# Kernel optimization log

Hardware: AMD Instinct MI355X
Metric: run time of the kernel (lower is better)

Reference implementation:

```python
import jax, jax.numpy as jnp
import numpy as np

B = 65536  # batch size


def setup_inputs() -> dict:
    key = jax.random.key(0)
    kx, kw, kb = jax.random.split(key, 3)
    x = jax.random.normal(kx, (B, 784), dtype=jnp.float32)
    W = jax.random.normal(kw, (10, 784), dtype=jnp.float32) * 0.03
    b = jax.random.normal(kb, (10,), dtype=jnp.float32) * 0.03
    return {"x": x, "W": W, "b": b}


def _quanv_features(x):
    # x: [B, 784] -> [B, 28, 28] -> 2x2 patches in row-major patch order,
    # each patch flattened as [p(r,c), p(r,c+1), p(r+1,c), p(r+1,c+1)].
    Bn = x.shape[0]
    p = x.reshape(Bn, 14, 2, 14, 2).transpose(0, 1, 3, 2, 4).reshape(Bn, 196, 4)
    # Analytic 4-qubit circuit: RY(x_i)|0>, CNOT(0,1), CNOT(2,3), <Z_i>
    # => [cos x0, cos x0 * cos x1, cos x2, cos x2 * cos x3]
    c = jnp.cos(p)
    m = jnp.stack(
        [c[..., 0], c[..., 0] * c[..., 1], c[..., 2], c[..., 2] * c[..., 3]],
        axis=-1,
    )
    # residual add with the raw patch, then concat over 196 patches -> [B, 784]
    return (m + p).reshape(Bn, 784)


def reference(x, W, b):
    feats = _quanv_features(x)              # [B, 784]
    logits = feats @ W.T + b                # [B, 10]
    return jax.nn.log_softmax(logits, axis=-1)
```

## Files before the change

### kernel.cpp

```cpp
#include <hip/hip_runtime.h>
#include <hip/hip_bf16.h>
#include <stdint.h>


typedef __attribute__((ext_vector_type(8))) short short8;
typedef __attribute__((ext_vector_type(4))) float f32x4;

__global__ void quanv_wprep_kernel(const float* __restrict__ Wm,
                                   uint32_t* __restrict__ ws) {
    const int idx = blockIdx.x * 256 + threadIdx.x;
    if (idx >= 7168) return;
    const int kb   = idx >> 8;
    const int rem  = idx & 255;
    const int l    = rem >> 2;
    const int d    = rem & 3;
    const int n    = l & 15;
    const int kg   = l >> 4;
    const int pr   = kb >> 1;
    const int half = kb & 1;
    uint32_t outv = 0;
    if (n < 10) {
        uint32_t hv[2];
#pragma unroll
        for (int d2 = 0; d2 < 2; ++d2) {
            const int e  = 2 * d + d2;
            const int fi = ((kg >= 2) ? 2 : 0) + (e & 1);
            int j; bool pad = false;
            if (half == 0) {
                j = 4 * (kg & 1) + (e >> 1);
            } else if ((kg & 1) == 0) {
                j = 8 + (e >> 1);
            } else {
                pad = (e < 4);
                const int e4 = (e >= 4) ? (e - 4) : 0;
                j = 12 + (e4 >> 1);
            }
            const float v = pad ? 0.f : Wm[n * 784 + (pr * 14 + j) * 4 + fi];
            hv[d2] = (uint32_t)__bfloat16_as_ushort(__float2bfloat16(v));
        }
        outv = hv[0] | (hv[1] << 16);
    }
    ws[idx] = outv;
}

#define QKB(P, IMM, WF) do {                                                  \
    const float4 va = *(const float4*)((P) + (IMM));                          \
    const float4 vb = *(const float4*)((P) + (IMM) + 4);                      \
    float g0,g1,g2,g3,g4,g5,g6,g7;                                            \
    { const float ce=__cosf(va.x), co=__cosf(va.y);                           \
      g0 = ce + va.x; g1 = fmaf(ce, co, va.y); }                              \
    { const float ce=__cosf(va.z), co=__cosf(va.w);                           \
      g2 = ce + va.z; g3 = fmaf(ce, co, va.w); }                              \
    { const float ce=__cosf(vb.x), co=__cosf(vb.y);                           \
      g4 = ce + vb.x; g5 = fmaf(ce, co, vb.y); }                              \
    { const float ce=__cosf(vb.z), co=__cosf(vb.w);                           \
      g6 = ce + vb.z; g7 = fmaf(ce, co, vb.w); }                              \
    short8 a;                                                                 \
    a[0]=(short)__bfloat16_as_ushort(__float2bfloat16(g0));                   \
    a[1]=(short)__bfloat16_as_ushort(__float2bfloat16(g1));                   \
    a[2]=(short)__bfloat16_as_ushort(__float2bfloat16(g2));                   \
    a[3]=(short)__bfloat16_as_ushort(__float2bfloat16(g3));                   \
    a[4]=(short)__bfloat16_as_ushort(__float2bfloat16(g4));                   \
    a[5]=(short)__bfloat16_as_ushort(__float2bfloat16(g5));                   \
    a[6]=(short)__bfloat16_as_ushort(__float2bfloat16(g6));                   \
    a[7]=(short)__bfloat16_as_ushort(__float2bfloat16(g7));                   \
    acc = __builtin_amdgcn_mfma_f32_16x16x32_bf16(a, (WF), acc, 0, 0, 0);     \
} while (0)

__global__ __launch_bounds__(256, 4)
void quanv_mfma3_kernel(const float* __restrict__ x,
                        const char* __restrict__ wsb,
                        const float* __restrict__ bias,
                        float* __restrict__ out) {
    __shared__ f32x4 red[2][64];

    const int t   = threadIdx.x;
    const int l   = t & 63;
    const int w   = t >> 6;
    const int rg  = __builtin_amdgcn_readfirstlane(w >> 1);
    const int kh  = __builtin_amdgcn_readfirstlane(w & 1);
    const int r16 = l & 15;
    const int kg  = l >> 4;
    const int rowBase = blockIdx.x * 32 + rg * 16;
    const float* xr = x + (size_t)(rowBase + r16) * 784 + kh * 392;

    const int off0 = (kg == 0) ? 0  : (kg == 1) ? 8  : (kg == 2) ? 28 : 36;
    const int off1 = (kg == 0) ? 16 : (kg == 1) ? 20 : (kg == 2) ? 44 : 48;
    const float* p0 = xr + off0;
    const float* p1 = xr + off1;

    const char* wbp = wsb + kh * 14336 + l * 16;
    const short8 wf0  = *(const short8*)(wbp + 0  * 1024);
    const short8 wf1  = *(const short8*)(wbp + 1  * 1024);
    const short8 wf2  = *(const short8*)(wbp + 2  * 1024);
    const short8 wf3  = *(const short8*)(wbp + 3  * 1024);
    const short8 wf4  = *(const short8*)(wbp + 4  * 1024);
    const short8 wf5  = *(const short8*)(wbp + 5  * 1024);
    const short8 wf6  = *(const short8*)(wbp + 6  * 1024);
    const short8 wf7  = *(const short8*)(wbp + 7  * 1024);
    const short8 wf8  = *(const short8*)(wbp + 8  * 1024);
    const short8 wf9  = *(const short8*)(wbp + 9  * 1024);
    const short8 wf10 = *(const short8*)(wbp + 10 * 1024);
    const short8 wf11 = *(const short8*)(wbp + 11 * 1024);
    const short8 wf12 = *(const short8*)(wbp + 12 * 1024);
    const short8 wf13 = *(const short8*)(wbp + 13 * 1024);

    f32x4 acc = {0.f, 0.f, 0.f, 0.f};

    QKB(p0, 0 * 56, wf0);  QKB(p1, 0 * 56, wf1);
    QKB(p0, 1 * 56, wf2);  QKB(p1, 1 * 56, wf3);
    QKB(p0, 2 * 56, wf4);  QKB(p1, 2 * 56, wf5);
    QKB(p0, 3 * 56, wf6);  QKB(p1, 3 * 56, wf7);
    QKB(p0, 4 * 56, wf8);  QKB(p1, 4 * 56, wf9);
    QKB(p0, 5 * 56, wf10); QKB(p1, 5 * 56, wf11);
    QKB(p0, 6 * 56, wf12); QKB(p1, 6 * 56, wf13);

    if (kh == 1) red[rg][l] = acc;
    __syncthreads();
    if (kh == 0) {
        const f32x4 o = red[rg][l];
#pragma unroll
        for (int j = 0; j < 4; ++j) acc[j] += o[j];

        const float bn = bias[r16 < 10 ? r16 : 0];
#pragma unroll
        for (int j = 0; j < 4; ++j) {
            float v = (r16 < 10) ? (acc[j] + bn) : -1e30f;
            float mx = v;
            mx = fmaxf(mx, __shfl_xor(mx, 1, 64));
            mx = fmaxf(mx, __shfl_xor(mx, 2, 64));
            mx = fmaxf(mx, __shfl_xor(mx, 4, 64));
            mx = fmaxf(mx, __shfl_xor(mx, 8, 64));
            float e = (r16 < 10) ? __expf(v - mx) : 0.f;
            float s = e;
            s += __shfl_xor(s, 1, 64);
            s += __shfl_xor(s, 2, 64);
            s += __shfl_xor(s, 4, 64);
            s += __shfl_xor(s, 8, 64);
            const float ls = __logf(s) + mx;
            if (r16 < 10)
                out[(size_t)(rowBase + 4 * kg + j) * 10 + r16] = v - ls;
        }
    }
}

extern "C" void kernel_launch(void* const* d_in, const int* in_sizes, int n_in,
                              void* d_out, int out_size, void* d_ws, size_t ws_size,
                              hipStream_t stream) {
    const float* x    = (const float*)d_in[0];
    const float* Wm   = (const float*)d_in[1];
    const float* bias = (const float*)d_in[2];
    float* out        = (float*)d_out;

    quanv_wprep_kernel<<<dim3(28), dim3(256), 0, stream>>>(
        Wm, (uint32_t*)d_ws);
    quanv_mfma3_kernel<<<dim3(2048), dim3(256), 0, stream>>>(
        x, (const char*)d_ws, bias, out);
}
```

Baseline: 45.92 us.

## Remap K dimension to contiguous 784-element layout removing padded MFMA steps

The K axis is re-indexed so each lane reads contiguous float4 pairs straight from the original row order, with the weight-prep kernel permuting W to match. This cuts the MFMA count from 28 to 25 K-tiles per row group by removing padding, and the tail tile reuses a valid in-row address (px) whose weights are zeroed. The two K-halves become unbalanced (13 vs 12 tiles), and the wider strided access pattern per lane changes coalescing.

```diff
diff --git a/kernel.cpp b/kernel.cpp
--- a/kernel.cpp
+++ b/kernel.cpp
@@ -9,33 +9,29 @@
 __global__ void quanv_wprep_kernel(const float* __restrict__ Wm,
                                    uint32_t* __restrict__ ws) {
     const int idx = blockIdx.x * 256 + threadIdx.x;
-    if (idx >= 7168) return;
-    const int kb   = idx >> 8;
-    const int rem  = idx & 255;
-    const int l    = rem >> 2;
-    const int d    = rem & 3;
-    const int n    = l & 15;
-    const int kg   = l >> 4;
-    const int pr   = kb >> 1;
-    const int half = kb & 1;
+    if (idx >= 6400) return;
+    const int kt  = idx >> 8;
+    const int rem = idx & 255;
+    const int l   = rem >> 2;
+    const int d   = rem & 3;
+    const int n   = l & 15;
+    const int kg  = l >> 4;
     uint32_t outv = 0;
     if (n < 10) {
         uint32_t hv[2];
 #pragma unroll
         for (int d2 = 0; d2 < 2; ++d2) {
             const int e  = 2 * d + d2;
-            const int fi = ((kg >= 2) ? 2 : 0) + (e & 1);
-            int j; bool pad = false;
-            if (half == 0) {
-                j = 4 * (kg & 1) + (e >> 1);
-            } else if ((kg & 1) == 0) {
-                j = 8 + (e >> 1);
-            } else {
-                pad = (e < 4);
-                const int e4 = (e >= 4) ? (e - 4) : 0;
-                j = 12 + (e4 >> 1);
+            const int jp = 32 * kt + 4 * kg + 16 * (e >> 2) + 2 * ((e >> 1) & 1);
+            float v = 0.f;
+            if (jp < 784) {
+                const int ri = jp / 28;
+                const int pc = (jp % 28) >> 1;
+                const int pr = ri >> 1;
+                const int ho = ri & 1;
+                const int col = (pr * 14 + pc) * 4 + 2 * ho + (e & 1);
+                v = Wm[n * 784 + col];
             }
-            const float v = pad ? 0.f : Wm[n * 784 + (pr * 14 + j) * 4 + fi];
             hv[d2] = (uint32_t)__bfloat16_as_ushort(__float2bfloat16(v));
         }
         outv = hv[0] | (hv[1] << 16);
@@ -43,32 +39,30 @@
     ws[idx] = outv;
 }
 
-#define QKB(P, IMM, WF) do {                                                  \
-    const float4 va = *(const float4*)((P) + (IMM));                          \
-    const float4 vb = *(const float4*)((P) + (IMM) + 4);                      \
-    float g0,g1,g2,g3,g4,g5,g6,g7;                                            \
-    { const float ce=__cosf(va.x), co=__cosf(va.y);                           \
-      g0 = ce + va.x; g1 = fmaf(ce, co, va.y); }                              \
-    { const float ce=__cosf(va.z), co=__cosf(va.w);                           \
-      g2 = ce + va.z; g3 = fmaf(ce, co, va.w); }                              \
-    { const float ce=__cosf(vb.x), co=__cosf(vb.y);                           \
-      g4 = ce + vb.x; g5 = fmaf(ce, co, vb.y); }                              \
-    { const float ce=__cosf(vb.z), co=__cosf(vb.w);                           \
-      g6 = ce + vb.z; g7 = fmaf(ce, co, vb.w); }                              \
-    short8 a;                                                                 \
-    a[0]=(short)__bfloat16_as_ushort(__float2bfloat16(g0));                   \
-    a[1]=(short)__bfloat16_as_ushort(__float2bfloat16(g1));                   \
-    a[2]=(short)__bfloat16_as_ushort(__float2bfloat16(g2));                   \
-    a[3]=(short)__bfloat16_as_ushort(__float2bfloat16(g3));                   \
-    a[4]=(short)__bfloat16_as_ushort(__float2bfloat16(g4));                   \
-    a[5]=(short)__bfloat16_as_ushort(__float2bfloat16(g5));                   \
-    a[6]=(short)__bfloat16_as_ushort(__float2bfloat16(g6));                   \
-    a[7]=(short)__bfloat16_as_ushort(__float2bfloat16(g7));                   \
+#define FEAT8(VA, VB, A) do {                                                 \
+    { const float ce=__cosf((VA).x), co=__cosf((VA).y);                       \
+      (A)[0]=(short)__bfloat16_as_ushort(__float2bfloat16(ce + (VA).x));      \
+      (A)[1]=(short)__bfloat16_as_ushort(__float2bfloat16(fmaf(ce,co,(VA).y)));}\
+    { const float ce=__cosf((VA).z), co=__cosf((VA).w);                       \
+      (A)[2]=(short)__bfloat16_as_ushort(__float2bfloat16(ce + (VA).z));      \
+      (A)[3]=(short)__bfloat16_as_ushort(__float2bfloat16(fmaf(ce,co,(VA).w)));}\
+    { const float ce=__cosf((VB).x), co=__cosf((VB).y);                       \
+      (A)[4]=(short)__bfloat16_as_ushort(__float2bfloat16(ce + (VB).x));      \
+      (A)[5]=(short)__bfloat16_as_ushort(__float2bfloat16(fmaf(ce,co,(VB).y)));}\
+    { const float ce=__cosf((VB).z), co=__cosf((VB).w);                       \
+      (A)[6]=(short)__bfloat16_as_ushort(__float2bfloat16(ce + (VB).z));      \
+      (A)[7]=(short)__bfloat16_as_ushort(__float2bfloat16(fmaf(ce,co,(VB).w)));}\
+} while (0)
+
+#define QKB(KT, WF) do {                                                      \
+    const float4 va = *(const float4*)(px + 32 * (KT));                       \
+    const float4 vb = *(const float4*)(px + 32 * (KT) + 16);                  \
+    short8 a; FEAT8(va, vb, a);                                               \
     acc = __builtin_amdgcn_mfma_f32_16x16x32_bf16(a, (WF), acc, 0, 0, 0);     \
 } while (0)
 
 __global__ __launch_bounds__(256, 4)
-void quanv_mfma3_kernel(const float* __restrict__ x,
+void quanv_mfma5_kernel(const float* __restrict__ x,
                         const char* __restrict__ wsb,
                         const float* __restrict__ bias,
                         float* __restrict__ out) {
@@ -82,38 +76,53 @@
     const int r16 = l & 15;
     const int kg  = l >> 4;
     const int rowBase = blockIdx.x * 32 + rg * 16;
-    const float* xr = x + (size_t)(rowBase + r16) * 784 + kh * 392;
-
-    const int off0 = (kg == 0) ? 0  : (kg == 1) ? 8  : (kg == 2) ? 28 : 36;
-    const int off1 = (kg == 0) ? 16 : (kg == 1) ? 20 : (kg == 2) ? 44 : 48;
-    const float* p0 = xr + off0;
-    const float* p1 = xr + off1;
-
-    const char* wbp = wsb + kh * 14336 + l * 16;
-    const short8 wf0  = *(const short8*)(wbp + 0  * 1024);
-    const short8 wf1  = *(const short8*)(wbp + 1  * 1024);
-    const short8 wf2  = *(const short8*)(wbp + 2  * 1024);
-    const short8 wf3  = *(const short8*)(wbp + 3  * 1024);
-    const short8 wf4  = *(const short8*)(wbp + 4  * 1024);
-    const short8 wf5  = *(const short8*)(wbp + 5  * 1024);
-    const short8 wf6  = *(const short8*)(wbp + 6  * 1024);
-    const short8 wf7  = *(const short8*)(wbp + 7  * 1024);
-    const short8 wf8  = *(const short8*)(wbp + 8  * 1024);
-    const short8 wf9  = *(const short8*)(wbp + 9  * 1024);
-    const short8 wf10 = *(const short8*)(wbp + 10 * 1024);
-    const short8 wf11 = *(const short8*)(wbp + 11 * 1024);
-    const short8 wf12 = *(const short8*)(wbp + 12 * 1024);
-    const short8 wf13 = *(const short8*)(wbp + 13 * 1024);
+    const float* px = x + (size_t)(rowBase + r16) * 784 + 4 * kg;
 
     f32x4 acc = {0.f, 0.f, 0.f, 0.f};
 
-    QKB(p0, 0 * 56, wf0);  QKB(p1, 0 * 56, wf1);
-    QKB(p0, 1 * 56, wf2);  QKB(p1, 1 * 56, wf3);
-    QKB(p0, 2 * 56, wf4);  QKB(p1, 2 * 56, wf5);
-    QKB(p0, 3 * 56, wf6);  QKB(p1, 3 * 56, wf7);
-    QKB(p0, 4 * 56, wf8);  QKB(p1, 4 * 56, wf9);
-    QKB(p0, 5 * 56, wf10); QKB(p1, 5 * 56, wf11);
-    QKB(p0, 6 * 56, wf12); QKB(p1, 6 * 56, wf13);
+    if (kh == 0) {
+        const char* wbp = wsb + l * 16;
+        const short8 wf0  = *(const short8*)(wbp + 0  * 1024);
+        const short8 wf1  = *(const short8*)(wbp + 1  * 1024);
+        const short8 wf2  = *(const short8*)(wbp + 2  * 1024);
+        const short8 wf3  = *(const short8*)(wbp + 3  * 1024);
+        const short8 wf4  = *(const short8*)(wbp + 4  * 1024);
+        const short8 wf5  = *(const short8*)(wbp + 5  * 1024);
+        const short8 wf6  = *(const short8*)(wbp + 6  * 1024);
+        const short8 wf7  = *(const short8*)(wbp + 7  * 1024);
+        const short8 wf8  = *(const short8*)(wbp + 8  * 1024);
+        const short8 wf9  = *(const short8*)(wbp + 9  * 1024);
+        const short8 wf10 = *(const short8*)(wbp + 10 * 1024);
+        const short8 wf11 = *(const short8*)(wbp + 11 * 1024);
+        const short8 wf12 = *(const short8*)(wbp + 12 * 1024);
+        QKB(0, wf0);  QKB(1, wf1);  QKB(2, wf2);  QKB(3, wf3);
+        QKB(4, wf4);  QKB(5, wf5);  QKB(6, wf6);  QKB(7, wf7);
+        QKB(8, wf8);  QKB(9, wf9);  QKB(10, wf10); QKB(11, wf11);
+        QKB(12, wf12);
+    } else {
+        const char* wbp = wsb + 13 * 1024 + l * 16;
+        const short8 wf0  = *(const short8*)(wbp + 0  * 1024);
+        const short8 wf1  = *(const short8*)(wbp + 1  * 1024);
+        const short8 wf2  = *(const short8*)(wbp + 2  * 1024);
+        const short8 wf3  = *(const short8*)(wbp + 3  * 1024);
+        const short8 wf4  = *(const short8*)(wbp + 4  * 1024);
+        const short8 wf5  = *(const short8*)(wbp + 5  * 1024);
+        const short8 wf6  = *(const short8*)(wbp + 6  * 1024);
+        const short8 wf7  = *(const short8*)(wbp + 7  * 1024);
+        const short8 wf8  = *(const short8*)(wbp + 8  * 1024);
+        const short8 wf9  = *(const short8*)(wbp + 9  * 1024);
+        const short8 wf10 = *(const short8*)(wbp + 10 * 1024);
+        const short8 wf11 = *(const short8*)(wbp + 11 * 1024);
+        QKB(13, wf0);  QKB(14, wf1);  QKB(15, wf2);  QKB(16, wf3);
+        QKB(17, wf4);  QKB(18, wf5);  QKB(19, wf6);  QKB(20, wf7);
+        QKB(21, wf8);  QKB(22, wf9);  QKB(23, wf10);
+        {
+            const float4 va = *(const float4*)(px + 32 * 24);
+            const float4 vb = *(const float4*)(px);
+            short8 a; FEAT8(va, vb, a);
+            acc = __builtin_amdgcn_mfma_f32_16x16x32_bf16(a, wf11, acc, 0, 0, 0);
+        }
+    }
 
     if (kh == 1) red[rg][l] = acc;
     __syncthreads();
@@ -152,8 +161,8 @@
     const float* bias = (const float*)d_in[2];
     float* out        = (float*)d_out;
 
-    quanv_wprep_kernel<<<dim3(28), dim3(256), 0, stream>>>(
+    quanv_wprep_kernel<<<dim3(25), dim3(256), 0, stream>>>(
         Wm, (uint32_t*)d_ws);
-    quanv_mfma3_kernel<<<dim3(2048), dim3(256), 0, stream>>>(
+    quanv_mfma5_kernel<<<dim3(2048), dim3(256), 0, stream>>>(
         x, (const char*)d_ws, bias, out);
 }
```

Measured after the change: 42.68 us. -7.0%, faster.
